# Optimization experiments

Measured on AMD Instinct MI355X. Metric: run time of the kernel, lower is better.

The kernel has to match this reference:

```python
import jax, jax.numpy as jnp
import numpy as np

SPATIAL_SHAPES = [(58, 100)]  # single level (H, W)
N_HEADS, N_LEVELS, N_POINTS, NUM_CAMS = 8, 1, 8, 6
D_MODEL = 256


def _bilinear_sample(v, loc, h, w):
    # v: (B, h, w, H, d); loc: (B, Lq, H, P, 2) normalized to [0,1]
    # matches F.grid_sample(mode='bilinear', padding_mode='zeros', align_corners=False)
    x = loc[..., 0] * w - 0.5
    y = loc[..., 1] * h - 0.5
    x0 = jnp.floor(x)
    y0 = jnp.floor(y)
    fx = x - x0
    fy = y - y0
    x0i = x0.astype(jnp.int32)
    y0i = y0.astype(jnp.int32)
    B, Hh = v.shape[0], v.shape[3]
    b = jnp.arange(B)[:, None, None, None]
    hd = jnp.arange(Hh)[None, None, :, None]

    def g(yi, xi):
        valid = ((yi >= 0) & (yi < h) & (xi >= 0) & (xi < w)).astype(v.dtype)
        yc = jnp.clip(yi, 0, h - 1)
        xc = jnp.clip(xi, 0, w - 1)
        return v[b, yc, xc, hd] * valid[..., None]  # (B,Lq,H,P,d)

    return (g(y0i, x0i) * ((1 - fy) * (1 - fx))[..., None]
            + g(y0i, x0i + 1) * ((1 - fy) * fx)[..., None]
            + g(y0i + 1, x0i) * (fy * (1 - fx))[..., None]
            + g(y0i + 1, x0i + 1) * (fy * fx)[..., None])


def _ms_deform_attn(value, locs, weights):
    # value: (B, S, H, d); locs: (B,Lq,H,L,P,2); weights: (B,Lq,H,L,P)
    B, S, Hh, d = value.shape
    out = 0.0
    start = 0
    for l, (h, w) in enumerate(SPATIAL_SHAPES):
        v = value[:, start:start + h * w].reshape(B, h, w, Hh, d)
        start += h * w
        samp = _bilinear_sample(v, locs[:, :, :, l], h, w)  # (B,Lq,H,P,d)
        out = out + jnp.einsum('bqhpd,bqhp->bqhd', samp, weights[:, :, :, l])
    return out.reshape(B, -1, Hh * d)


def setup_inputs() -> dict:
    key = jax.random.key(0)
    ks = jax.random.split(key, 12)
    B, Lq, C = 1, 22500, D_MODEL
    S = sum(h * w for h, w in SPATIAL_SHAPES)
    inp = {
        'query': jax.random.normal(ks[0], (B, Lq, C), jnp.float32),
        'reference_points_cam': jax.random.uniform(ks[1], (NUM_CAMS, B, Lq, 4, 2), jnp.float32),
        'bev_mask': jax.random.randint(ks[2], (NUM_CAMS, B, Lq, 4), 0, 2, jnp.int32),
        'value': jax.random.normal(ks[3], (B * NUM_CAMS, S, C), jnp.float32),
        'W_off': jax.random.normal(ks[4], (N_HEADS * N_LEVELS * N_POINTS * 2, C), jnp.float32) * 0.01,
        'b_off': jax.random.normal(ks[5], (N_HEADS * N_LEVELS * N_POINTS * 2,), jnp.float32),
        'W_attn': jax.random.normal(ks[6], (N_HEADS * N_LEVELS * N_POINTS, C), jnp.float32) * 0.02,
        'b_attn': jnp.zeros((N_HEADS * N_LEVELS * N_POINTS,), jnp.float32),
        'W_val': jax.random.normal(ks[7], (C, C), jnp.float32) * (1.0 / np.sqrt(C)),
        'b_val': jnp.zeros((C,), jnp.float32),
        'W_out': jax.random.normal(ks[8], (C, C), jnp.float32) * (1.0 / np.sqrt(C)),
        'b_out': jnp.zeros((C,), jnp.float32),
    }
    return inp


def reference(query, reference_points_cam, bev_mask, value,
              W_off, b_off, W_attn, b_attn, W_val, b_val, W_out, b_out):
    B, Lq, C = query.shape
    d = C // N_HEADS
    D = reference_points_cam.shape[3]  # num_Z_anchors = 4
    S = value.shape[1]

    # value_proj for all cameras; value rows are laid out as b*num_cams + cam
    val = value @ W_val.T + b_val
    val = val.reshape(B, NUM_CAMS, S, N_HEADS, d).transpose(1, 0, 2, 3, 4)  # (cams,B,S,H,d)

    # query-side projections are camera-independent
    off = (query @ W_off.T + b_off).reshape(B, Lq, N_HEADS, N_LEVELS, N_POINTS, 2)
    normalizer = jnp.array([[w, h] for (h, w) in SPATIAL_SHAPES], dtype=query.dtype)  # (L,2)
    off = off / normalizer[None, None, None, :, None, :]
    off = off.reshape(B, Lq, N_HEADS, N_LEVELS, N_POINTS // D, D, 2)

    aw = (query @ W_attn.T + b_attn).reshape(B, Lq, N_HEADS, N_LEVELS * N_POINTS)
    aw = jax.nn.softmax(aw, axis=-1).reshape(B, Lq, N_HEADS, N_LEVELS, N_POINTS)

    vis = (bev_mask.sum(-1) > 0)  # (cams, B, Lq)
    slots = jnp.zeros_like(query)
    for cam in range(NUM_CAMS):  # small fixed camera set
        ref = reference_points_cam[cam][:, :, None, None, None, :, :]  # (B,Lq,1,1,1,D,2)
        locs = (ref + off).reshape(B, Lq, N_HEADS, N_LEVELS, N_POINTS, 2)
        out = _ms_deform_attn(val[cam], locs, aw)  # (B,Lq,C)
        slots = slots + out * vis[cam][..., None].astype(query.dtype)

    count = jnp.maximum(vis.sum(0).astype(query.dtype), 1.0)  # (B,Lq)
    slots = slots / count[..., None]
    return slots @ W_out.T + b_out
```

## Files before the change

kernel.cpp:

```cpp
#include <hip/hip_runtime.h>

#define LQ     22500
#define SPA_H  58
#define SPA_W  100
#define S_TOT  5800
#define NCAMS  6
#define CDIM   256

typedef __attribute__((ext_vector_type(8))) _Float16 half8;
typedef __attribute__((ext_vector_type(4))) _Float16 half4;
typedef __attribute__((ext_vector_type(4))) float f32x4;

__global__ __launch_bounds__(256) void cvt_all(
    const float* __restrict__ value, const float* __restrict__ query,
    const float* __restrict__ W_val, const float* __restrict__ W_off,
    const float* __restrict__ W_attn, const float* __restrict__ W_out,
    _Float16* __restrict__ val16, _Float16* __restrict__ q16,
    _Float16* __restrict__ Wv, _Float16* __restrict__ Wcat,
    _Float16* __restrict__ Wo) {
  const long long e = ((long long)blockIdx.x * 256 + threadIdx.x) * 4;
  const float* src; _Float16* dst; long long off;
  if (e < 8908800)        { src = value;  dst = val16;        off = e; }
  else if (e < 14668800)  { src = query;  dst = q16;          off = e - 8908800; }
  else if (e < 14734336)  { src = W_val;  dst = Wv;           off = e - 14668800; }
  else if (e < 14767104)  { src = W_off;  dst = Wcat;         off = e - 14734336; }
  else if (e < 14783488)  { src = W_attn; dst = Wcat + 32768; off = e - 14767104; }
  else if (e < 14849024)  { src = W_out;  dst = Wo;           off = e - 14783488; }
  else return;
  f32x4 v = *(const f32x4*)(src + off);
  half4 o;
  o[0] = (_Float16)v.x; o[1] = (_Float16)v.y; o[2] = (_Float16)v.z; o[3] = (_Float16)v.w;
  *(half4*)(dst + off) = o;
}

template<int N, int OUT_MODE, bool INPLACE>
__device__ __forceinline__ void gemm_body(
    const _Float16* __restrict__ A, const _Float16* __restrict__ W,
    const float* __restrict__ bias, const float* __restrict__ bias2,
    void* __restrict__ Cv, int M, int rowbase) {
  constexpr int NT = N / 64;
  const int lane = threadIdx.x & 63;
  const int wave = threadIdx.x >> 6;
  const int m15  = lane & 15;
  const int quad = lane >> 4;
  const int colbase = wave * (N / 4);
  const int kq = quad * 8;

  const _Float16* ap[4];
#pragma unroll
  for (int rt = 0; rt < 4; ++rt) {
    int r = rowbase + rt * 16 + m15;
    r = r < M ? r : M - 1;
    ap[rt] = A + (size_t)r * 256 + kq;
  }
  const _Float16* wp[NT];
#pragma unroll
  for (int t = 0; t < NT; ++t)
    wp[t] = W + (size_t)(colbase + t * 16 + m15) * 256 + kq;

  f32x4 acc[4][NT];
#pragma unroll
  for (int rt = 0; rt < 4; ++rt)
#pragma unroll
    for (int t = 0; t < NT; ++t) acc[rt][t] = (f32x4){0.f, 0.f, 0.f, 0.f};

  half8 a0[4], b0[NT], a1[4], b1[NT];
#define LOADSET(aa, bb, KO) \
  { _Pragma("unroll") for (int rt = 0; rt < 4; ++rt) aa[rt] = *(const half8*)(ap[rt] + (KO)); \
    _Pragma("unroll") for (int t = 0; t < NT; ++t)  bb[t]  = *(const half8*)(wp[t] + (KO)); }
#define MFMASET(aa, bb) \
  { _Pragma("unroll") for (int t = 0; t < NT; ++t) \
      _Pragma("unroll") for (int rt = 0; rt < 4; ++rt) \
        acc[rt][t] = __builtin_amdgcn_mfma_f32_16x16x32_f16(aa[rt], bb[t], acc[rt][t], 0, 0, 0); }

  LOADSET(a0, b0, 0)
#pragma unroll 1
  for (int kk = 0; kk < 192; kk += 64) {
    LOADSET(a1, b1, kk + 32)
    MFMASET(a0, b0)
    LOADSET(a0, b0, kk + 64)
    MFMASET(a1, b1)
  }
  LOADSET(a1, b1, 224)
  MFMASET(a0, b0)
  MFMASET(a1, b1)
#undef LOADSET
#undef MFMASET

  if (INPLACE) __syncthreads();

#pragma unroll
  for (int rt = 0; rt < 4; ++rt) {
    const int orow = rowbase + rt * 16 + quad * 4;
#pragma unroll
    for (int t = 0; t < NT; ++t) {
      const int col = colbase + t * 16 + m15;
      const float bv = (N == 192 && col >= 128) ? bias2[col - 128] : bias[col];
#pragma unroll
      for (int i = 0; i < 4; ++i) {
        const int r = orow + i;
        if (r < M) {
          const float v = acc[rt][t][i] + bv;
          if (OUT_MODE == 0) ((float*)Cv)[(size_t)r * 256 + col] = v;
          else               ((_Float16*)Cv)[(size_t)r * 256 + col] = (_Float16)v;
        }
      }
    }
  }
}

__global__ __launch_bounds__(256) void gemm_inputs(
    const _Float16* __restrict__ val16, const _Float16* __restrict__ q16,
    const _Float16* __restrict__ Wv, const _Float16* __restrict__ Wcat,
    const float* __restrict__ b_val, const float* __restrict__ b_off,
    const float* __restrict__ b_attn,
    _Float16* __restrict__ vp, _Float16* __restrict__ qproj) {
  const int b = blockIdx.x;
  if (b < 544) gemm_body<256, 2, true>(val16, Wv, b_val, b_val, vp, 34800, b * 64);
  else         gemm_body<192, 2, true>(q16, Wcat, b_off, b_attn, qproj, LQ, (b - 544) * 64);
}

__global__ __launch_bounds__(256) void gemm_out_k(
    const _Float16* __restrict__ slots, const _Float16* __restrict__ Wo,
    const float* __restrict__ b_out, float* __restrict__ out) {
  gemm_body<256, 0, false>(slots, Wo, b_out, b_out, out, LQ, blockIdx.x * 64);
}

__global__ __launch_bounds__(128) void sampler(
    const _Float16* __restrict__ vp,
    const _Float16* __restrict__ qproj,
    const float* __restrict__ ref,
    const int* __restrict__ bev,
    _Float16* __restrict__ slots)
{
  const int t  = threadIdx.x;
  const int ql = t >> 4;
  const int s  = t & 15;
  const int h  = s >> 1;
  const int q  = blockIdx.x * 8 + ql;
  const bool qok = q < LQ;

  __shared__ float s_off[8][8][17];
  __shared__ float s_w8[8][8][9];
  __shared__ float s_ref[8][48];
  __shared__ int   s_vis[8][6];

  if (qok) {
    const _Float16* qp = qproj + (size_t)q * 256;
    {
      half8 oc = *(const half8*)(qp + s * 8);
#pragma unroll
      for (int i = 0; i < 8; ++i) {
        const int f = s * 8 + i;
        s_off[ql][f >> 4][f & 15] =
            (float)oc[i] * ((f & 1) ? (1.f / 58.f) : (1.f / 100.f));
      }
    }
    if (s < 8) {
      half8 aw = *(const half8*)(qp + 128 + s * 8);
      float m = -1e30f;
#pragma unroll
      for (int p = 0; p < 8; ++p) m = fmaxf(m, (float)aw[p]);
      float e[8], ssum = 0.f;
#pragma unroll
      for (int p = 0; p < 8; ++p) { e[p] = __expf((float)aw[p] - m); ssum += e[p]; }
      const float inv = 1.f / ssum;
#pragma unroll
      for (int p = 0; p < 8; ++p) s_w8[ql][s][p] = e[p] * inv;
    }
    if (s < 12) {
      const int cam = s >> 1, hf = s & 1;
      f32x4 r = *(const f32x4*)(ref + ((size_t)cam * LQ + q) * 8 + hf * 4);
      *(f32x4*)&s_ref[ql][s * 4] = r;
    }
    if (s < 6) {
      int4 bm = *(const int4*)(bev + ((size_t)s * LQ + q) * 4);
      s_vis[ql][s] = (bm.x + bm.y + bm.z + bm.w) > 0 ? 1 : 0;
    }
  }
  __syncthreads();
  if (!qok) return;

  int cnt = 0;
#pragma unroll
  for (int c = 0; c < 6; ++c) cnt += s_vis[ql][c];
  const float invc = 1.f / (float)(cnt > 0 ? cnt : 1);

  float acc[16];
#pragma unroll
  for (int i = 0; i < 16; ++i) acc[i] = 0.f;

#pragma unroll 1
  for (int cam = 0; cam < NCAMS; ++cam) {
    if (!s_vis[ql][cam]) continue;
    const _Float16* vpc = vp + (size_t)cam * (S_TOT * CDIM) + s * 16;

#pragma unroll 1
    for (int pp = 0; pp < 4; ++pp) {
      half8 v[16];
      float w[8];
#pragma unroll
      for (int j = 0; j < 2; ++j) {
        const int p = pp * 2 + j;
        const int z = p & 3;
        const float x = (s_ref[ql][cam * 8 + z * 2 + 0] + s_off[ql][h][p * 2 + 0]) * 100.f - 0.5f;
        const float y = (s_ref[ql][cam * 8 + z * 2 + 1] + s_off[ql][h][p * 2 + 1]) * 58.f - 0.5f;
        const float x0f = floorf(x), y0f = floorf(y);
        const float fx = x - x0f, fy = y - y0f;
        const int x0 = (int)x0f, y0 = (int)y0f;
        const float vx0 = (x0 >= 0 && x0 < SPA_W) ? 1.f : 0.f;
        const float vx1 = (x0 >= -1 && x0 < SPA_W - 1) ? 1.f : 0.f;
        const float vy0 = (y0 >= 0 && y0 < SPA_H) ? 1.f : 0.f;
        const float vy1 = (y0 >= -1 && y0 < SPA_H - 1) ? 1.f : 0.f;
        const int xc0 = min(max(x0, 0), SPA_W - 1), xc1 = min(max(x0 + 1, 0), SPA_W - 1);
        const int yc0 = min(max(y0, 0), SPA_H - 1), yc1 = min(max(y0 + 1, 0), SPA_H - 1);
        const float wgt = s_w8[ql][h][p];
        const float wy0 = (1.f - fy) * wgt, wy1 = fy * wgt;
        w[j * 4 + 0] = wy0 * (1.f - fx) * vy0 * vx0;
        w[j * 4 + 1] = wy0 * fx * vy0 * vx1;
        w[j * 4 + 2] = wy1 * (1.f - fx) * vy1 * vx0;
        w[j * 4 + 3] = wy1 * fx * vy1 * vx1;
        const _Float16* t00 = vpc + (size_t)(yc0 * SPA_W + xc0) * CDIM;
        const _Float16* t01 = vpc + (size_t)(yc0 * SPA_W + xc1) * CDIM;
        const _Float16* t10 = vpc + (size_t)(yc1 * SPA_W + xc0) * CDIM;
        const _Float16* t11 = vpc + (size_t)(yc1 * SPA_W + xc1) * CDIM;
        v[j * 8 + 0] = *(const half8*)t00; v[j * 8 + 1] = *(const half8*)(t00 + 8);
        v[j * 8 + 2] = *(const half8*)t01; v[j * 8 + 3] = *(const half8*)(t01 + 8);
        v[j * 8 + 4] = *(const half8*)t10; v[j * 8 + 5] = *(const half8*)(t10 + 8);
        v[j * 8 + 6] = *(const half8*)t11; v[j * 8 + 7] = *(const half8*)(t11 + 8);
      }
#pragma unroll
      for (int j = 0; j < 2; ++j)
#pragma unroll
        for (int tap = 0; tap < 4; ++tap) {
          const float wk = w[j * 4 + tap];
#pragma unroll
          for (int i = 0; i < 8; ++i) {
            acc[i]     = fmaf(wk, (float)v[j * 8 + tap * 2][i],     acc[i]);
            acc[8 + i] = fmaf(wk, (float)v[j * 8 + tap * 2 + 1][i], acc[8 + i]);
          }
        }
    }
  }

  half8 o0, o1;
#pragma unroll
  for (int i = 0; i < 8; ++i) {
    o0[i] = (_Float16)(acc[i] * invc);
    o1[i] = (_Float16)(acc[8 + i] * invc);
  }
  _Float16* sp = slots + (size_t)q * 256 + s * 16;
  *(half8*)sp = o0;
  *(half8*)(sp + 8) = o1;
}

extern "C" void kernel_launch(void* const* d_in, const int* in_sizes, int n_in,
                              void* d_out, int out_size, void* d_ws, size_t ws_size,
                              hipStream_t stream) {
  const float* query  = (const float*)d_in[0];
  const float* refpts = (const float*)d_in[1];
  const int*   bev    = (const int*)d_in[2];
  const float* value  = (const float*)d_in[3];
  const float* W_off  = (const float*)d_in[4];
  const float* b_off  = (const float*)d_in[5];
  const float* W_attn = (const float*)d_in[6];
  const float* b_attn = (const float*)d_in[7];
  const float* W_val  = (const float*)d_in[8];
  const float* b_val  = (const float*)d_in[9];
  const float* W_out  = (const float*)d_in[10];
  const float* b_out  = (const float*)d_in[11];

  char* ws = (char*)d_ws;
  _Float16* val16 = (_Float16*)(ws + 0);
  _Float16* q16   = (_Float16*)(ws + 17817600);
  _Float16* Wv    = (_Float16*)(ws + 29337600);
  _Float16* Wcat  = (_Float16*)(ws + 29468672);
  _Float16* Wo    = (_Float16*)(ws + 29566976);

  cvt_all<<<14501, 256, 0, stream>>>(value, query, W_val, W_off, W_attn, W_out,
                                     val16, q16, Wv, Wcat, Wo);

  gemm_inputs<<<896, 256, 0, stream>>>(val16, q16, Wv, Wcat,
                                       b_val, b_off, b_attn, val16, q16);

  sampler<<<(LQ + 7) / 8, 128, 0, stream>>>(val16, q16, refpts, bev, q16);

  gemm_out_k<<<(LQ + 63) / 64, 256, 0, stream>>>(q16, Wo, b_out, (float*)d_out);
}
```

Measured before the change: 408.4 us.

## Fuse fp32-to-fp16 activation conversion into input GEMMs and restructure sampler loop

The activation conversion pass is removed: the input GEMMs now load fp32 value and query rows directly and convert them to fp16 in registers before the MFMA, so only the weights are converted ahead of time. This drops a full read/write pass over roughly 15M elements, and with it the in-place sync. The sampler no longer branches per camera on visibility. Instead it multiplies the visibility into the weights and fully unrolls all 8 points, giving the compiler more memory-level parallelism at the cost of doing work for invisible cameras. Launch bounds are set to 2 blocks per CU for the GEMMs, and the fp32 A loads double register use there.

```diff
diff --git a/kernel.cpp b/kernel.cpp
--- a/kernel.cpp
+++ b/kernel.cpp
@@ -11,21 +11,24 @@
 typedef __attribute__((ext_vector_type(4))) _Float16 half4;
 typedef __attribute__((ext_vector_type(4))) float f32x4;
 
-__global__ __launch_bounds__(256) void cvt_all(
-    const float* __restrict__ value, const float* __restrict__ query,
+__device__ __forceinline__ half8 cvt8(f32x4 lo, f32x4 hi) {
+  half8 r;
+  r[0] = (_Float16)lo.x; r[1] = (_Float16)lo.y; r[2] = (_Float16)lo.z; r[3] = (_Float16)lo.w;
+  r[4] = (_Float16)hi.x; r[5] = (_Float16)hi.y; r[6] = (_Float16)hi.z; r[7] = (_Float16)hi.w;
+  return r;
+}
+
+__global__ __launch_bounds__(256) void cvt_w(
     const float* __restrict__ W_val, const float* __restrict__ W_off,
     const float* __restrict__ W_attn, const float* __restrict__ W_out,
-    _Float16* __restrict__ val16, _Float16* __restrict__ q16,
     _Float16* __restrict__ Wv, _Float16* __restrict__ Wcat,
     _Float16* __restrict__ Wo) {
-  const long long e = ((long long)blockIdx.x * 256 + threadIdx.x) * 4;
-  const float* src; _Float16* dst; long long off;
-  if (e < 8908800)        { src = value;  dst = val16;        off = e; }
-  else if (e < 14668800)  { src = query;  dst = q16;          off = e - 8908800; }
-  else if (e < 14734336)  { src = W_val;  dst = Wv;           off = e - 14668800; }
-  else if (e < 14767104)  { src = W_off;  dst = Wcat;         off = e - 14734336; }
-  else if (e < 14783488)  { src = W_attn; dst = Wcat + 32768; off = e - 14767104; }
-  else if (e < 14849024)  { src = W_out;  dst = Wo;           off = e - 14783488; }
+  const int e = (blockIdx.x * 256 + threadIdx.x) * 4;
+  const float* src; _Float16* dst; int off;
+  if (e < 65536)       { src = W_val;  dst = Wv;   off = e; }
+  else if (e < 98304)  { src = W_off;  dst = Wcat; off = e - 65536; }
+  else if (e < 114688) { src = W_attn; dst = Wcat + 32768; off = e - 98304; }
+  else if (e < 180224) { src = W_out;  dst = Wo;   off = e - 114688; }
   else return;
   f32x4 v = *(const f32x4*)(src + off);
   half4 o;
@@ -33,11 +36,11 @@
   *(half4*)(dst + off) = o;
 }
 
-template<int N, int OUT_MODE, bool INPLACE>
-__device__ __forceinline__ void gemm_body(
-    const _Float16* __restrict__ A, const _Float16* __restrict__ W,
+template<int N>
+__device__ __forceinline__ void gemm_body_af32(
+    const float* __restrict__ A, const _Float16* __restrict__ W,
     const float* __restrict__ bias, const float* __restrict__ bias2,
-    void* __restrict__ Cv, int M, int rowbase) {
+    _Float16* __restrict__ C, int M, int rowbase) {
   constexpr int NT = N / 64;
   const int lane = threadIdx.x & 63;
   const int wave = threadIdx.x >> 6;
@@ -46,7 +49,7 @@
   const int colbase = wave * (N / 4);
   const int kq = quad * 8;
 
-  const _Float16* ap[4];
+  const float* ap[4];
 #pragma unroll
   for (int rt = 0; rt < 4; ++rt) {
     int r = rowbase + rt * 16 + m15;
@@ -64,14 +67,101 @@
 #pragma unroll
     for (int t = 0; t < NT; ++t) acc[rt][t] = (f32x4){0.f, 0.f, 0.f, 0.f};
 
+  f32x4 al0[4], ah0[4], al1[4], ah1[4];
+  half8 b0[NT], b1[NT];
+
+#define LOADSET(AL, AH, BB, KO) \
+  { _Pragma("unroll") for (int rt = 0; rt < 4; ++rt) { \
+      AL[rt] = *(const f32x4*)(ap[rt] + (KO)); \
+      AH[rt] = *(const f32x4*)(ap[rt] + (KO) + 4); } \
+    _Pragma("unroll") for (int t = 0; t < NT; ++t) \
+      BB[t] = *(const half8*)(wp[t] + (KO)); }
+#define MFMASET(AL, AH, BB) \
+  { half8 af[4]; \
+    _Pragma("unroll") for (int rt = 0; rt < 4; ++rt) af[rt] = cvt8(AL[rt], AH[rt]); \
+    _Pragma("unroll") for (int t = 0; t < NT; ++t) \
+      _Pragma("unroll") for (int rt = 0; rt < 4; ++rt) \
+        acc[rt][t] = __builtin_amdgcn_mfma_f32_16x16x32_f16(af[rt], BB[t], acc[rt][t], 0, 0, 0); }
+
+  LOADSET(al0, ah0, b0, 0)
+#pragma unroll 1
+  for (int kk = 0; kk < 192; kk += 64) {
+    LOADSET(al1, ah1, b1, kk + 32)
+    MFMASET(al0, ah0, b0)
+    LOADSET(al0, ah0, b0, kk + 64)
+    MFMASET(al1, ah1, b1)
+  }
+  LOADSET(al1, ah1, b1, 224)
+  MFMASET(al0, ah0, b0)
+  MFMASET(al1, ah1, b1)
+#undef LOADSET
+#undef MFMASET
+
+#pragma unroll
+  for (int rt = 0; rt < 4; ++rt) {
+    const int orow = rowbase + rt * 16 + quad * 4;
+#pragma unroll
+    for (int t = 0; t < NT; ++t) {
+      const int col = colbase + t * 16 + m15;
+      const float bv = (N == 192 && col >= 128) ? bias2[col - 128] : bias[col];
+#pragma unroll
+      for (int i = 0; i < 4; ++i) {
+        const int r = orow + i;
+        if (r < M) C[(size_t)r * 256 + col] = (_Float16)(acc[rt][t][i] + bv);
+      }
+    }
+  }
+}
+
+__global__ __launch_bounds__(256, 2) void gemm_inputs(
+    const float* __restrict__ value, const float* __restrict__ query,
+    const _Float16* __restrict__ Wv, const _Float16* __restrict__ Wcat,
+    const float* __restrict__ b_val, const float* __restrict__ b_off,
+    const float* __restrict__ b_attn,
+    _Float16* __restrict__ vp, _Float16* __restrict__ qproj) {
+  const int b = blockIdx.x;
+  if (b < 544) gemm_body_af32<256>(value, Wv, b_val, b_val, vp, 34800, b * 64);
+  else         gemm_body_af32<192>(query, Wcat, b_off, b_attn, qproj, LQ, (b - 544) * 64);
+}
+
+__global__ __launch_bounds__(256, 2) void gemm_out_k(
+    const _Float16* __restrict__ A, const _Float16* __restrict__ W,
+    const float* __restrict__ bias, float* __restrict__ out) {
+  constexpr int NT = 4;
+  const int lane = threadIdx.x & 63;
+  const int wave = threadIdx.x >> 6;
+  const int m15  = lane & 15;
+  const int quad = lane >> 4;
+  const int rowbase = blockIdx.x * 64;
+  const int colbase = wave * 64;
+  const int kq = quad * 8;
+
+  const _Float16* ap[4];
+#pragma unroll
+  for (int rt = 0; rt < 4; ++rt) {
+    int r = rowbase + rt * 16 + m15;
+    r = r < LQ ? r : LQ - 1;
+    ap[rt] = A + (size_t)r * 256 + kq;
+  }
+  const _Float16* wp[NT];
+#pragma unroll
+  for (int t = 0; t < NT; ++t)
+    wp[t] = W + (size_t)(colbase + t * 16 + m15) * 256 + kq;
+
+  f32x4 acc[4][NT];
+#pragma unroll
+  for (int rt = 0; rt < 4; ++rt)
+#pragma unroll
+    for (int t = 0; t < NT; ++t) acc[rt][t] = (f32x4){0.f, 0.f, 0.f, 0.f};
+
   half8 a0[4], b0[NT], a1[4], b1[NT];
-#define LOADSET(aa, bb, KO) \
-  { _Pragma("unroll") for (int rt = 0; rt < 4; ++rt) aa[rt] = *(const half8*)(ap[rt] + (KO)); \
-    _Pragma("unroll") for (int t = 0; t < NT; ++t)  bb[t]  = *(const half8*)(wp[t] + (KO)); }
-#define MFMASET(aa, bb) \
+#define LOADSET(AA, BB, KO) \
+  { _Pragma("unroll") for (int rt = 0; rt < 4; ++rt) AA[rt] = *(const half8*)(ap[rt] + (KO)); \
+    _Pragma("unroll") for (int t = 0; t < NT; ++t)  BB[t]  = *(const half8*)(wp[t] + (KO)); }
+#define MFMASET(AA, BB) \
   { _Pragma("unroll") for (int t = 0; t < NT; ++t) \
       _Pragma("unroll") for (int rt = 0; rt < 4; ++rt) \
-        acc[rt][t] = __builtin_amdgcn_mfma_f32_16x16x32_f16(aa[rt], bb[t], acc[rt][t], 0, 0, 0); }
+        acc[rt][t] = __builtin_amdgcn_mfma_f32_16x16x32_f16(AA[rt], BB[t], acc[rt][t], 0, 0, 0); }
 
   LOADSET(a0, b0, 0)
 #pragma unroll 1
@@ -87,43 +177,20 @@
 #undef LOADSET
 #undef MFMASET
 
-  if (INPLACE) __syncthreads();
-
 #pragma unroll
   for (int rt = 0; rt < 4; ++rt) {
     const int orow = rowbase + rt * 16 + quad * 4;
 #pragma unroll
     for (int t = 0; t < NT; ++t) {
       const int col = colbase + t * 16 + m15;
-      const float bv = (N == 192 && col >= 128) ? bias2[col - 128] : bias[col];
+      const float bv = bias[col];
 #pragma unroll
       for (int i = 0; i < 4; ++i) {
         const int r = orow + i;
-        if (r < M) {
-          const float v = acc[rt][t][i] + bv;
-          if (OUT_MODE == 0) ((float*)Cv)[(size_t)r * 256 + col] = v;
-          else               ((_Float16*)Cv)[(size_t)r * 256 + col] = (_Float16)v;
-        }
+        if (r < LQ) out[(size_t)r * 256 + col] = acc[rt][t][i] + bv;
       }
     }
   }
-}
-
-__global__ __launch_bounds__(256) void gemm_inputs(
-    const _Float16* __restrict__ val16, const _Float16* __restrict__ q16,
-    const _Float16* __restrict__ Wv, const _Float16* __restrict__ Wcat,
-    const float* __restrict__ b_val, const float* __restrict__ b_off,
-    const float* __restrict__ b_attn,
-    _Float16* __restrict__ vp, _Float16* __restrict__ qproj) {
-  const int b = blockIdx.x;
-  if (b < 544) gemm_body<256, 2, true>(val16, Wv, b_val, b_val, vp, 34800, b * 64);
-  else         gemm_body<192, 2, true>(q16, Wcat, b_off, b_attn, qproj, LQ, (b - 544) * 64);
-}
-
-__global__ __launch_bounds__(256) void gemm_out_k(
-    const _Float16* __restrict__ slots, const _Float16* __restrict__ Wo,
-    const float* __restrict__ b_out, float* __restrict__ out) {
-  gemm_body<256, 0, false>(slots, Wo, b_out, b_out, out, LQ, blockIdx.x * 64);
 }
 
 __global__ __launch_bounds__(128) void sampler(
@@ -143,8 +210,9 @@
   __shared__ float s_off[8][8][17];
   __shared__ float s_w8[8][8][9];
   __shared__ float s_ref[8][48];
-  __shared__ int   s_vis[8][6];
-
+  __shared__ float s_vis[8][6];
+
+  if (s < 6) s_vis[ql][s] = 0.f;
   if (qok) {
     const _Float16* qp = qproj + (size_t)q * 256;
     {
@@ -175,16 +243,20 @@
     }
     if (s < 6) {
       int4 bm = *(const int4*)(bev + ((size_t)s * LQ + q) * 4);
-      s_vis[ql][s] = (bm.x + bm.y + bm.z + bm.w) > 0 ? 1 : 0;
+      s_vis[ql][s] = (bm.x + bm.y + bm.z + bm.w) > 0 ? 1.f : 0.f;
     }
   }
   __syncthreads();
   if (!qok) return;
 
-  int cnt = 0;
+  float cnt = 0.f;
 #pragma unroll
   for (int c = 0; c < 6; ++c) cnt += s_vis[ql][c];
-  const float invc = 1.f / (float)(cnt > 0 ? cnt : 1);
+  const float invc = 1.f / fmaxf(cnt, 1.f);
+
+  float w8r[8];
+#pragma unroll
+  for (int p = 0; p < 8; ++p) w8r[p] = s_w8[ql][h][p];
 
   float acc[16];
 #pragma unroll
@@ -192,54 +264,52 @@
 
 #pragma unroll 1
   for (int cam = 0; cam < NCAMS; ++cam) {
-    if (!s_vis[ql][cam]) continue;
+    const float visf = s_vis[ql][cam];
     const _Float16* vpc = vp + (size_t)cam * (S_TOT * CDIM) + s * 16;
-
-#pragma unroll 1
-    for (int pp = 0; pp < 4; ++pp) {
-      half8 v[16];
-      float w[8];
-#pragma unroll
-      for (int j = 0; j < 2; ++j) {
-        const int p = pp * 2 + j;
-        const int z = p & 3;
-        const float x = (s_ref[ql][cam * 8 + z * 2 + 0] + s_off[ql][h][p * 2 + 0]) * 100.f - 0.5f;
-        const float y = (s_ref[ql][cam * 8 + z * 2 + 1] + s_off[ql][h][p * 2 + 1]) * 58.f - 0.5f;
-        const float x0f = floorf(x), y0f = floorf(y);
-        const float fx = x - x0f, fy = y - y0f;
-        const int x0 = (int)x0f, y0 = (int)y0f;
-        const float vx0 = (x0 >= 0 && x0 < SPA_W) ? 1.f : 0.f;
-        const float vx1 = (x0 >= -1 && x0 < SPA_W - 1) ? 1.f : 0.f;
-        const float vy0 = (y0 >= 0 && y0 < SPA_H) ? 1.f : 0.f;
-        const float vy1 = (y0 >= -1 && y0 < SPA_H - 1) ? 1.f : 0.f;
-        const int xc0 = min(max(x0, 0), SPA_W - 1), xc1 = min(max(x0 + 1, 0), SPA_W - 1);
-        const int yc0 = min(max(y0, 0), SPA_H - 1), yc1 = min(max(y0 + 1, 0), SPA_H - 1);
-        const float wgt = s_w8[ql][h][p];
-        const float wy0 = (1.f - fy) * wgt, wy1 = fy * wgt;
-        w[j * 4 + 0] = wy0 * (1.f - fx) * vy0 * vx0;
-        w[j * 4 + 1] = wy0 * fx * vy0 * vx1;
-        w[j * 4 + 2] = wy1 * (1.f - fx) * vy1 * vx0;
-        w[j * 4 + 3] = wy1 * fx * vy1 * vx1;
-        const _Float16* t00 = vpc + (size_t)(yc0 * SPA_W + xc0) * CDIM;
-        const _Float16* t01 = vpc + (size_t)(yc0 * SPA_W + xc1) * CDIM;
-        const _Float16* t10 = vpc + (size_t)(yc1 * SPA_W + xc0) * CDIM;
-        const _Float16* t11 = vpc + (size_t)(yc1 * SPA_W + xc1) * CDIM;
-        v[j * 8 + 0] = *(const half8*)t00; v[j * 8 + 1] = *(const half8*)(t00 + 8);
-        v[j * 8 + 2] = *(const half8*)t01; v[j * 8 + 3] = *(const half8*)(t01 + 8);
-        v[j * 8 + 4] = *(const half8*)t10; v[j * 8 + 5] = *(const half8*)(t10 + 8);
-        v[j * 8 + 6] = *(const half8*)t11; v[j * 8 + 7] = *(const half8*)(t11 + 8);
+    float cx[4], cy[4];
+#pragma unroll
+    for (int z = 0; z < 4; ++z) {
+      cx[z] = s_ref[ql][cam * 8 + z * 2 + 0];
+      cy[z] = s_ref[ql][cam * 8 + z * 2 + 1];
+    }
+#pragma unroll
+    for (int p = 0; p < 8; ++p) {
+      const int z = p & 3;
+      const float x = (cx[z] + s_off[ql][h][p * 2 + 0]) * 100.f - 0.5f;
+      const float y = (cy[z] + s_off[ql][h][p * 2 + 1]) * 58.f - 0.5f;
+      const float x0f = floorf(x), y0f = floorf(y);
+      const float fx = x - x0f, fy = y - y0f;
+      const int x0 = (int)x0f, y0 = (int)y0f;
+      const float vx0 = (x0 >= 0 && x0 < SPA_W) ? 1.f : 0.f;
+      const float vx1 = (x0 >= -1 && x0 < SPA_W - 1) ? 1.f : 0.f;
+      const float vy0 = (y0 >= 0 && y0 < SPA_H) ? 1.f : 0.f;
+      const float vy1 = (y0 >= -1 && y0 < SPA_H - 1) ? 1.f : 0.f;
+      const int xc0 = min(max(x0, 0), SPA_W - 1), xc1 = min(max(x0 + 1, 0), SPA_W - 1);
+      const int yc0 = min(max(y0, 0), SPA_H - 1), yc1 = min(max(y0 + 1, 0), SPA_H - 1);
+      const float wgt = w8r[p] * visf;
+      const float wy0 = (1.f - fy) * vy0 * wgt, wy1 = fy * vy1 * wgt;
+      const float bx0 = (1.f - fx) * vx0,       bx1 = fx * vx1;
+      const float w00 = wy0 * bx0, w01 = wy0 * bx1;
+      const float w10 = wy1 * bx0, w11 = wy1 * bx1;
+      const _Float16* t00 = vpc + (size_t)(yc0 * SPA_W + xc0) * CDIM;
+      const _Float16* t01 = vpc + (size_t)(yc0 * SPA_W + xc1) * CDIM;
+      const _Float16* t10 = vpc + (size_t)(yc1 * SPA_W + xc0) * CDIM;
+      const _Float16* t11 = vpc + (size_t)(yc1 * SPA_W + xc1) * CDIM;
+      half8 v00a = *(const half8*)t00, v00b = *(const half8*)(t00 + 8);
+      half8 v01a = *(const half8*)t01, v01b = *(const half8*)(t01 + 8);
+      half8 v10a = *(const half8*)t10, v10b = *(const half8*)(t10 + 8);
+      half8 v11a = *(const half8*)t11, v11b = *(const half8*)(t11 + 8);
+#pragma unroll
+      for (int i = 0; i < 8; ++i) {
+        acc[i]     = fmaf(w00, (float)v00a[i], acc[i]);
+        acc[8 + i] = fmaf(w00, (float)v00b[i], acc[8 + i]);
+        acc[i]     = fmaf(w01, (float)v01a[i], acc[i]);
+        acc[8 + i] = fmaf(w01, (float)v01b[i], acc[8 + i]);
+        acc[i]     = fmaf(w10, (float)v10a[i], acc[i]);
+        acc[8 + i] = fmaf(w10, (float)v10b[i], acc[8 + i]);
+        acc[i]     = fmaf(w11, (float)v11a[i], acc[i]);
+        acc[8 + i] = fmaf(w11, (float)v11b[i], acc[8 + i]);
       }
-#pragma unroll
-      for (int j = 0; j < 2; ++j)
-#pragma unroll
-        for (int tap = 0; tap < 4; ++tap) {
-          const float wk = w[j * 4 + tap];
-#pragma unroll
-          for (int i = 0; i < 8; ++i) {
-            acc[i]     = fmaf(wk, (float)v[j * 8 + tap * 2][i],     acc[i]);
-            acc[8 + i] = fmaf(wk, (float)v[j * 8 + tap * 2 + 1][i], acc[8 + i]);
-          }
-        }
     }
   }
 
@@ -271,19 +341,18 @@
   const float* b_out  = (const float*)d_in[11];
 
   char* ws = (char*)d_ws;
-  _Float16* val16 = (_Float16*)(ws + 0);
-  _Float16* q16   = (_Float16*)(ws + 17817600);
+  _Float16* vp    = (_Float16*)(ws + 0);
+  _Float16* qproj = (_Float16*)(ws + 17817600);
   _Float16* Wv    = (_Float16*)(ws + 29337600);
   _Float16* Wcat  = (_Float16*)(ws + 29468672);
   _Float16* Wo    = (_Float16*)(ws + 29566976);
 
-  cvt_all<<<14501, 256, 0, stream>>>(value, query, W_val, W_off, W_attn, W_out,
-                                     val16, q16, Wv, Wcat, Wo);
-
-  gemm_inputs<<<896, 256, 0, stream>>>(val16, q16, Wv, Wcat,
-                                       b_val, b_off, b_attn, val16, q16);
-
-  sampler<<<(LQ + 7) / 8, 128, 0, stream>>>(val16, q16, refpts, bev, q16);
-
-  gemm_out_k<<<(LQ + 63) / 64, 256, 0, stream>>>(q16, Wo, b_out, (float*)d_out);
-}
+  cvt_w<<<176, 256, 0, stream>>>(W_val, W_off, W_attn, W_out, Wv, Wcat, Wo);
+
+  gemm_inputs<<<896, 256, 0, stream>>>(value, query, Wv, Wcat,
+                                       b_val, b_off, b_attn, vp, qproj);
+
+  sampler<<<(LQ + 7) / 8, 128, 0, stream>>>(vp, qproj, refpts, bev, qproj);
+
+  gemm_out_k<<<(LQ + 63) / 64, 256, 0, stream>>>(qproj, Wo, b_out, (float*)d_out);
+}
```

New measurement: 470.4 us. 1.15x slower.
